# Optimization experiments

Hardware: AMD Instinct MI355X
Metric: run time of the kernel (lower is better)

Reference implementation:

```python
import jax, jax.numpy as jnp
import numpy as np

B, N = 4096, 2048


def _nrmse(o, t):
    # o, t: [B, 1, N]. Per-sample RMSE over all non-batch elements,
    # normalized by per-sample (max - min) of the target.
    rmse = jnp.sqrt(jnp.mean((o - t) ** 2, axis=(1, 2)))        # [B]
    rng = jnp.max(t, axis=(1, 2)) - jnp.min(t, axis=(1, 2))     # [B]
    return rmse / rng


def setup_inputs() -> dict:
    key = jax.random.key(0)
    ks = jax.random.split(key, 6)
    names = ["o1", "t1", "o2", "t2", "o3", "t3"]
    return {n: jax.random.normal(k, (B, 1, N), dtype=jnp.float32) for n, k in zip(names, ks)}


def reference(o1, t1, o2, t2, o3, t3):
    loss = (0.5 * _nrmse(o1, t1)
            + 0.25 * _nrmse(o2, t2)
            + 0.25 * _nrmse(o3, t3))  # [B]
    return jnp.mean(loss)
```

## Files before the change

### kernel.cpp

```cpp
#include <hip/hip_runtime.h>
#include <math.h>

constexpr int N_ELEM = 2048;
constexpr int BATCH  = 4096;
constexpr int BLOCK  = 256;
constexpr int TASKS  = 3 * BATCH;
constexpr int GRID1  = TASKS / (BLOCK / 64);

__global__ __launch_bounds__(BLOCK)
void wnrmse_stage1(const float* __restrict__ o1, const float* __restrict__ t1,
                   const float* __restrict__ o2, const float* __restrict__ t2,
                   const float* __restrict__ o3, const float* __restrict__ t3,
                   float* __restrict__ partial)
{
    const int tid  = threadIdx.x;
    const int wave = tid >> 6;
    const int lane = tid & 63;
    const int task = blockIdx.x * (BLOCK / 64) + wave;

    const int pair = task >> 12;
    const int row  = task & (BATCH - 1);

    const float* ob = (pair == 0) ? o1 : ((pair == 1) ? o2 : o3);
    const float* tb = (pair == 0) ? t1 : ((pair == 1) ? t2 : t3);
    const float  wgt = (pair == 0) ? 0.50f : 0.25f;

    const float4* o4 = (const float4*)(ob + (size_t)row * N_ELEM);
    const float4* t4 = (const float4*)(tb + (size_t)row * N_ELEM);

    float ssd0 = 0.0f, ssd1 = 0.0f;
    float tmax0 = -INFINITY, tmax1 = -INFINITY;
    float tmin0 =  INFINITY, tmin1 =  INFINITY;

#pragma unroll
    for (int j = 0; j < (N_ELEM / 4) / 64; ++j) {
        const int i = lane + j * 64;
        float4 ov = o4[i];
        float4 tv = t4[i];
        float d0 = ov.x - tv.x;
        float d1 = ov.y - tv.y;
        float d2 = ov.z - tv.z;
        float d3 = ov.w - tv.w;
        ssd0 += d0 * d0 + d1 * d1;
        ssd1 += d2 * d2 + d3 * d3;
        tmax0 = fmaxf(tmax0, fmaxf(tv.x, tv.y));
        tmax1 = fmaxf(tmax1, fmaxf(tv.z, tv.w));
        tmin0 = fminf(tmin0, fminf(tv.x, tv.y));
        tmin1 = fminf(tmin1, fminf(tv.z, tv.w));
    }
    float ssd  = ssd0 + ssd1;
    float tmax = fmaxf(tmax0, tmax1);
    float tmin = fminf(tmin0, tmin1);

#pragma unroll
    for (int off = 32; off > 0; off >>= 1) {
        ssd  += __shfl_xor(ssd, off, 64);
        tmax  = fmaxf(tmax, __shfl_xor(tmax, off, 64));
        tmin  = fminf(tmin, __shfl_xor(tmin, off, 64));
    }

    const float rmse  = sqrtf(ssd * (1.0f / (float)N_ELEM));
    const float local = wgt * rmse / (tmax - tmin);

    __shared__ float s_part[BLOCK / 64];
    if (lane == 0) s_part[wave] = local;
    __syncthreads();
    if (tid == 0) {
        partial[blockIdx.x] = s_part[0] + s_part[1] + s_part[2] + s_part[3];
    }
}

__global__ __launch_bounds__(BLOCK)
void wnrmse_stage2(const float* __restrict__ partial, float* __restrict__ out)
{
    const int tid = threadIdx.x;
    float s = 0.0f;
    for (int i = tid; i < GRID1; i += BLOCK) s += partial[i];

#pragma unroll
    for (int off = 32; off > 0; off >>= 1) s += __shfl_xor(s, off, 64);

    __shared__ float s_part[BLOCK / 64];
    const int wave = tid >> 6;
    const int lane = tid & 63;
    if (lane == 0) s_part[wave] = s;
    __syncthreads();
    if (tid == 0) {
        float tot = s_part[0] + s_part[1] + s_part[2] + s_part[3];
        out[0] = tot * (1.0f / (float)BATCH);
    }
}

extern "C" void kernel_launch(void* const* d_in, const int* in_sizes, int n_in,
                              void* d_out, int out_size, void* d_ws, size_t ws_size,
                              hipStream_t stream) {
    const float* o1 = (const float*)d_in[0];
    const float* t1 = (const float*)d_in[1];
    const float* o2 = (const float*)d_in[2];
    const float* t2 = (const float*)d_in[3];
    const float* o3 = (const float*)d_in[4];
    const float* t3 = (const float*)d_in[5];
    float* out     = (float*)d_out;
    float* partial = (float*)d_ws;

    wnrmse_stage1<<<GRID1, BLOCK, 0, stream>>>(o1, t1, o2, t2, o3, t3, partial);
    wnrmse_stage2<<<1, BLOCK, 0, stream>>>(partial, out);
}
```

Before: 205.5 us.

## Make stage1 persistent with double-buffered inline-asm row loads

The stage-1 grid shrinks to 768 blocks, and each wave now handles four rows instead of one. Rows are fetched with inline-asm global_load_dwordx4 bursts into two register sets, and explicit s_waitcnt vmcnt gating lets the next row's loads run while the current row is reduced. The aim is more memory-level parallelism per wave and less block launch and tail overhead in this bandwidth-bound reduction. The cost is heavy register use (launch_bounds 3), lower occupancy, and fragile hand-written waitcnt ordering.

```diff
diff --git a/kernel.cpp b/kernel.cpp
--- a/kernel.cpp
+++ b/kernel.cpp
@@ -5,9 +5,80 @@
 constexpr int BATCH  = 4096;
 constexpr int BLOCK  = 256;
 constexpr int TASKS  = 3 * BATCH;
-constexpr int GRID1  = TASKS / (BLOCK / 64);
+constexpr int GRID1  = 768;
+constexpr int WAVES  = GRID1 * (BLOCK/64);
+static_assert(TASKS % WAVES == 0, "tasks must divide evenly");
 
-__global__ __launch_bounds__(BLOCK)
+typedef float f32x4 __attribute__((ext_vector_type(4)));
+
+#define DECL_SET(P) f32x4 P##o0,P##o1,P##o2,P##o3,P##o4,P##o5,P##o6,P##o7, \
+                          P##t0,P##t1,P##t2,P##t3,P##t4,P##t5,P##t6,P##t7;
+
+#define BURST(P, OLO, OHI, TLO, THI)                                        \
+    asm volatile(                                                           \
+        "global_load_dwordx4 %0,  %[olo], off\n\t"                          \
+        "global_load_dwordx4 %1,  %[olo], off offset:1024\n\t"              \
+        "global_load_dwordx4 %2,  %[olo], off offset:2048\n\t"              \
+        "global_load_dwordx4 %3,  %[olo], off offset:3072\n\t"              \
+        "global_load_dwordx4 %4,  %[ohi], off\n\t"                          \
+        "global_load_dwordx4 %5,  %[ohi], off offset:1024\n\t"              \
+        "global_load_dwordx4 %6,  %[ohi], off offset:2048\n\t"              \
+        "global_load_dwordx4 %7,  %[ohi], off offset:3072\n\t"              \
+        "global_load_dwordx4 %8,  %[tlo], off\n\t"                          \
+        "global_load_dwordx4 %9,  %[tlo], off offset:1024\n\t"              \
+        "global_load_dwordx4 %10, %[tlo], off offset:2048\n\t"              \
+        "global_load_dwordx4 %11, %[tlo], off offset:3072\n\t"              \
+        "global_load_dwordx4 %12, %[thi], off\n\t"                          \
+        "global_load_dwordx4 %13, %[thi], off offset:1024\n\t"              \
+        "global_load_dwordx4 %14, %[thi], off offset:2048\n\t"              \
+        "global_load_dwordx4 %15, %[thi], off offset:3072"                  \
+        : "=&v"(P##o0), "=&v"(P##o1), "=&v"(P##o2), "=&v"(P##o3),           \
+          "=&v"(P##o4), "=&v"(P##o5), "=&v"(P##o6), "=&v"(P##o7),           \
+          "=&v"(P##t0), "=&v"(P##t1), "=&v"(P##t2), "=&v"(P##t3),           \
+          "=&v"(P##t4), "=&v"(P##t5), "=&v"(P##t6), "=&v"(P##t7)            \
+        : [olo] "v"(OLO), [ohi] "v"(OHI), [tlo] "v"(TLO), [thi] "v"(THI)    \
+        : "memory");
+
+#define WAITV16 asm volatile("s_waitcnt vmcnt(16)" ::: "memory"); \
+                __builtin_amdgcn_sched_barrier(0);
+#define WAITV0  asm volatile("s_waitcnt vmcnt(0)"  ::: "memory"); \
+                __builtin_amdgcn_sched_barrier(0);
+
+#define ACC(OV, TV)                                                  \
+    {                                                                \
+        float d0 = OV[0] - TV[0];                                    \
+        float d1 = OV[1] - TV[1];                                    \
+        float d2 = OV[2] - TV[2];                                    \
+        float d3 = OV[3] - TV[3];                                    \
+        ssd0 += d0 * d0 + d1 * d1;                                   \
+        ssd1 += d2 * d2 + d3 * d3;                                   \
+        tmax0 = fmaxf(tmax0, fmaxf(TV[0], TV[1]));                   \
+        tmax1 = fmaxf(tmax1, fmaxf(TV[2], TV[3]));                   \
+        tmin0 = fminf(tmin0, fminf(TV[0], TV[1]));                   \
+        tmin1 = fminf(tmin1, fminf(TV[2], TV[3]));                   \
+    }
+
+#define ROWSTAT(P, W)                                                       \
+    {                                                                       \
+        float ssd0 = 0.0f, ssd1 = 0.0f;                                     \
+        float tmax0 = -INFINITY, tmax1 = -INFINITY;                         \
+        float tmin0 =  INFINITY, tmin1 =  INFINITY;                         \
+        ACC(P##o0, P##t0) ACC(P##o1, P##t1) ACC(P##o2, P##t2)               \
+        ACC(P##o3, P##t3) ACC(P##o4, P##t4) ACC(P##o5, P##t5)               \
+        ACC(P##o6, P##t6) ACC(P##o7, P##t7)                                 \
+        float ssd  = ssd0 + ssd1;                                           \
+        float tmax = fmaxf(tmax0, tmax1);                                   \
+        float tmin = fminf(tmin0, tmin1);                                   \
+        _Pragma("unroll")                                                   \
+        for (int off = 32; off > 0; off >>= 1) {                            \
+            ssd  += __shfl_xor(ssd, off, 64);                               \
+            tmax  = fmaxf(tmax, __shfl_xor(tmax, off, 64));                 \
+            tmin  = fminf(tmin, __shfl_xor(tmin, off, 64));                 \
+        }                                                                   \
+        local += (W) * sqrtf(ssd * (1.0f / (float)N_ELEM)) / (tmax - tmin); \
+    }
+
+__global__ __launch_bounds__(BLOCK, 3)
 void wnrmse_stage1(const float* __restrict__ o1, const float* __restrict__ t1,
                    const float* __restrict__ o2, const float* __restrict__ t2,
                    const float* __restrict__ o3, const float* __restrict__ t3,
@@ -16,51 +87,46 @@
     const int tid  = threadIdx.x;
     const int wave = tid >> 6;
     const int lane = tid & 63;
-    const int task = blockIdx.x * (BLOCK / 64) + wave;
+    const int gw   = blockIdx.x * (BLOCK / 64) + wave;
 
-    const int pair = task >> 12;
-    const int row  = task & (BATCH - 1);
+    struct Addr { const float* olo; const float* ohi;
+                  const float* tlo; const float* thi; float w; };
+    auto decode = [&](int task, Addr& a) {
+        const int pair = task >> 12;
+        const int row  = task & (BATCH - 1);
+        const float* ob = (pair == 0) ? o1 : ((pair == 1) ? o2 : o3);
+        const float* tb = (pair == 0) ? t1 : ((pair == 1) ? t2 : t3);
+        a.olo = ob + (size_t)row * N_ELEM + lane * 4;
+        a.ohi = a.olo + 1024;
+        a.tlo = tb + (size_t)row * N_ELEM + lane * 4;
+        a.thi = a.tlo + 1024;
+        a.w   = (pair == 0) ? 0.50f : 0.25f;
+    };
 
-    const float* ob = (pair == 0) ? o1 : ((pair == 1) ? o2 : o3);
-    const float* tb = (pair == 0) ? t1 : ((pair == 1) ? t2 : t3);
-    const float  wgt = (pair == 0) ? 0.50f : 0.25f;
+    float local = 0.0f;
+    DECL_SET(A) DECL_SET(B) DECL_SET(C) DECL_SET(D)
 
-    const float4* o4 = (const float4*)(ob + (size_t)row * N_ELEM);
-    const float4* t4 = (const float4*)(tb + (size_t)row * N_ELEM);
+    Addr k0, k1, k2, k3;
+    decode(gw,             k0);
+    decode(gw + WAVES,     k1);
+    BURST(A, k0.olo, k0.ohi, k0.tlo, k0.thi)
+    BURST(B, k1.olo, k1.ohi, k1.tlo, k1.thi)
 
-    float ssd0 = 0.0f, ssd1 = 0.0f;
-    float tmax0 = -INFINITY, tmax1 = -INFINITY;
-    float tmin0 =  INFINITY, tmin1 =  INFINITY;
+    WAITV16
+    ROWSTAT(A, k0.w)
+    decode(gw + 2 * WAVES, k2);
+    BURST(C, k2.olo, k2.ohi, k2.tlo, k2.thi)
 
-#pragma unroll
-    for (int j = 0; j < (N_ELEM / 4) / 64; ++j) {
-        const int i = lane + j * 64;
-        float4 ov = o4[i];
-        float4 tv = t4[i];
-        float d0 = ov.x - tv.x;
-        float d1 = ov.y - tv.y;
-        float d2 = ov.z - tv.z;
-        float d3 = ov.w - tv.w;
-        ssd0 += d0 * d0 + d1 * d1;
-        ssd1 += d2 * d2 + d3 * d3;
-        tmax0 = fmaxf(tmax0, fmaxf(tv.x, tv.y));
-        tmax1 = fmaxf(tmax1, fmaxf(tv.z, tv.w));
-        tmin0 = fminf(tmin0, fminf(tv.x, tv.y));
-        tmin1 = fminf(tmin1, fminf(tv.z, tv.w));
-    }
-    float ssd  = ssd0 + ssd1;
-    float tmax = fmaxf(tmax0, tmax1);
-    float tmin = fminf(tmin0, tmin1);
+    WAITV16
+    ROWSTAT(B, k1.w)
+    decode(gw + 3 * WAVES, k3);
+    BURST(D, k3.olo, k3.ohi, k3.tlo, k3.thi)
 
-#pragma unroll
-    for (int off = 32; off > 0; off >>= 1) {
-        ssd  += __shfl_xor(ssd, off, 64);
-        tmax  = fmaxf(tmax, __shfl_xor(tmax, off, 64));
-        tmin  = fminf(tmin, __shfl_xor(tmin, off, 64));
-    }
+    WAITV16
+    ROWSTAT(C, k2.w)
 
-    const float rmse  = sqrtf(ssd * (1.0f / (float)N_ELEM));
-    const float local = wgt * rmse / (tmax - tmin);
+    WAITV0
+    ROWSTAT(D, k3.w)
 
     __shared__ float s_part[BLOCK / 64];
     if (lane == 0) s_part[wave] = local;
```

Result: slower. 212.5 us (+3.4%).

## Use persistent waves with double-buffered inline-asm loads across rows

Applied to the files above, without the earlier changes.

Replaces one-row-per-wave blocks with a fixed grid of 512 blocks in which each wave handles several rows. Each row is split into two halves loaded with inline-asm global_load_dwordx4 bursts, and the next row's loads are issued while the current half is being computed, with explicit vmcnt waits. A block-index swizzle spreads consecutive rows across blocks. The aim is to keep more memory requests in flight per wave and hide load latency on a bandwidth-bound reduction. The cost is high register use and fragile hand-written waitcnt ordering.

```diff
diff --git a/kernel.cpp b/kernel.cpp
--- a/kernel.cpp
+++ b/kernel.cpp
@@ -5,9 +5,53 @@
 constexpr int BATCH  = 4096;
 constexpr int BLOCK  = 256;
 constexpr int TASKS  = 3 * BATCH;
-constexpr int GRID1  = TASKS / (BLOCK / 64);
+constexpr int GRID1  = 512;
+constexpr int WAVES  = GRID1 * (BLOCK / 64);
+constexpr int TPW    = TASKS / WAVES;
+static_assert(TASKS % WAVES == 0, "tasks must divide evenly");
 
-__global__ __launch_bounds__(BLOCK)
+typedef float f32x4 __attribute__((ext_vector_type(4)));
+
+#define DECL8(P) f32x4 P##o0, P##o1, P##o2, P##o3, P##t0, P##t1, P##t2, P##t3;
+
+#define BURST8(P, OB, TB)                                                   \
+    asm volatile(                                                           \
+        "global_load_dwordx4 %0, %[ob], off\n\t"                            \
+        "global_load_dwordx4 %1, %[ob], off offset:1024\n\t"                \
+        "global_load_dwordx4 %2, %[ob], off offset:2048\n\t"                \
+        "global_load_dwordx4 %3, %[ob], off offset:3072\n\t"                \
+        "global_load_dwordx4 %4, %[tb], off\n\t"                            \
+        "global_load_dwordx4 %5, %[tb], off offset:1024\n\t"                \
+        "global_load_dwordx4 %6, %[tb], off offset:2048\n\t"                \
+        "global_load_dwordx4 %7, %[tb], off offset:3072"                    \
+        : "=&v"(P##o0), "=&v"(P##o1), "=&v"(P##o2), "=&v"(P##o3),           \
+          "=&v"(P##t0), "=&v"(P##t1), "=&v"(P##t2), "=&v"(P##t3)            \
+        : [ob] "v"(OB), [tb] "v"(TB)                                        \
+        : "memory");
+
+#define WAITV8 asm volatile("s_waitcnt vmcnt(8)" ::: "memory"); \
+               __builtin_amdgcn_sched_barrier(0);
+#define WAITV0 asm volatile("s_waitcnt vmcnt(0)" ::: "memory"); \
+               __builtin_amdgcn_sched_barrier(0);
+
+#define ACC(OV, TV)                                                  \
+    {                                                                \
+        float d0 = OV[0] - TV[0];                                    \
+        float d1 = OV[1] - TV[1];                                    \
+        float d2 = OV[2] - TV[2];                                    \
+        float d3 = OV[3] - TV[3];                                    \
+        ssd0 += d0 * d0 + d1 * d1;                                   \
+        ssd1 += d2 * d2 + d3 * d3;                                   \
+        mx0 = fmaxf(mx0, fmaxf(TV[0], TV[1]));                       \
+        mx1 = fmaxf(mx1, fmaxf(TV[2], TV[3]));                       \
+        mn0 = fminf(mn0, fminf(TV[0], TV[1]));                       \
+        mn1 = fminf(mn1, fminf(TV[2], TV[3]));                       \
+    }
+
+#define COMPUTE8(P) ACC(P##o0, P##t0) ACC(P##o1, P##t1) \
+                    ACC(P##o2, P##t2) ACC(P##o3, P##t3)
+
+__global__ __launch_bounds__(BLOCK, 1)
 void wnrmse_stage1(const float* __restrict__ o1, const float* __restrict__ t1,
                    const float* __restrict__ o2, const float* __restrict__ t2,
                    const float* __restrict__ o3, const float* __restrict__ t3,
@@ -16,51 +60,64 @@
     const int tid  = threadIdx.x;
     const int wave = tid >> 6;
     const int lane = tid & 63;
-    const int task = blockIdx.x * (BLOCK / 64) + wave;
 
-    const int pair = task >> 12;
-    const int row  = task & (BATCH - 1);
+    const int bid  = (int)blockIdx.x;
+    const int swz  = (bid & 7) * (GRID1 / 8) + (bid >> 3);
+    const int gw   = swz * (BLOCK / 64) + wave;
+    const int base = gw * TPW;
 
-    const float* ob = (pair == 0) ? o1 : ((pair == 1) ? o2 : o3);
-    const float* tb = (pair == 0) ? t1 : ((pair == 1) ? t2 : t3);
-    const float  wgt = (pair == 0) ? 0.50f : 0.25f;
+    struct Addr { const float* olo; const float* ohi;
+                  const float* tlo; const float* thi; float w; };
+    auto decode = [&](int task, Addr& a) {
+        const int pair = task >> 12;
+        const int row  = task & (BATCH - 1);
+        const float* ob = (pair == 0) ? o1 : ((pair == 1) ? o2 : o3);
+        const float* tb = (pair == 0) ? t1 : ((pair == 1) ? t2 : t3);
+        a.olo = ob + (size_t)row * N_ELEM + lane * 4;
+        a.ohi = a.olo + 1024;
+        a.tlo = tb + (size_t)row * N_ELEM + lane * 4;
+        a.thi = a.tlo + 1024;
+        a.w   = (pair == 0) ? 0.50f : 0.25f;
+    };
 
-    const float4* o4 = (const float4*)(ob + (size_t)row * N_ELEM);
-    const float4* t4 = (const float4*)(tb + (size_t)row * N_ELEM);
+    float local = 0.0f;
+    DECL8(A) DECL8(B)
 
-    float ssd0 = 0.0f, ssd1 = 0.0f;
-    float tmax0 = -INFINITY, tmax1 = -INFINITY;
-    float tmin0 =  INFINITY, tmin1 =  INFINITY;
+    Addr k, kn;
+    decode(base, k);
+    BURST8(A, k.olo, k.tlo)
+    BURST8(B, k.ohi, k.thi)
 
 #pragma unroll
-    for (int j = 0; j < (N_ELEM / 4) / 64; ++j) {
-        const int i = lane + j * 64;
-        float4 ov = o4[i];
-        float4 tv = t4[i];
-        float d0 = ov.x - tv.x;
-        float d1 = ov.y - tv.y;
-        float d2 = ov.z - tv.z;
-        float d3 = ov.w - tv.w;
-        ssd0 += d0 * d0 + d1 * d1;
-        ssd1 += d2 * d2 + d3 * d3;
-        tmax0 = fmaxf(tmax0, fmaxf(tv.x, tv.y));
-        tmax1 = fmaxf(tmax1, fmaxf(tv.z, tv.w));
-        tmin0 = fminf(tmin0, fminf(tv.x, tv.y));
-        tmin1 = fminf(tmin1, fminf(tv.z, tv.w));
+    for (int i = 0; i < TPW; ++i) {
+        if (i + 1 < TPW) decode(base + i + 1, kn);
+
+        float ssd0 = 0.0f, ssd1 = 0.0f;
+        float mx0 = -INFINITY, mx1 = -INFINITY;
+        float mn0 =  INFINITY, mn1 =  INFINITY;
+
+        WAITV8
+        COMPUTE8(A)
+        if (i + 1 < TPW) BURST8(A, kn.olo, kn.tlo)
+
+        if (i + 1 < TPW) { WAITV8 }
+        else             { WAITV0 }
+        COMPUTE8(B)
+        if (i + 1 < TPW) BURST8(B, kn.ohi, kn.thi)
+
+        float ssd = ssd0 + ssd1;
+        float mx  = fmaxf(mx0, mx1);
+        float mn  = fminf(mn0, mn1);
+#pragma unroll
+        for (int off = 32; off > 0; off >>= 1) {
+            ssd += __shfl_xor(ssd, off, 64);
+            mx   = fmaxf(mx, __shfl_xor(mx, off, 64));
+            mn   = fminf(mn, __shfl_xor(mn, off, 64));
+        }
+        local += k.w * sqrtf(ssd * (1.0f / (float)N_ELEM)) / (mx - mn);
+
+        k = kn;
     }
-    float ssd  = ssd0 + ssd1;
-    float tmax = fmaxf(tmax0, tmax1);
-    float tmin = fminf(tmin0, tmin1);
-
-#pragma unroll
-    for (int off = 32; off > 0; off >>= 1) {
-        ssd  += __shfl_xor(ssd, off, 64);
-        tmax  = fmaxf(tmax, __shfl_xor(tmax, off, 64));
-        tmin  = fminf(tmin, __shfl_xor(tmin, off, 64));
-    }
-
-    const float rmse  = sqrtf(ssd * (1.0f / (float)N_ELEM));
-    const float local = wgt * rmse / (tmax - tmin);
 
     __shared__ float s_part[BLOCK / 64];
     if (lane == 0) s_part[wave] = local;
```

After: 211.5 us. 2.9% more time.
